# Kernel optimization log

Hardware: AMD Instinct MI355X
Metric: run time of the kernel (lower is better)

Reference implementation:

```python
import jax, jax.numpy as jnp
import numpy as np

HEADS = 16
EMB_DIM = 1024
MODEL_DIM = 1024
HEAD_DIM = EMB_DIM // HEADS
N, SEQ = 4, 1024


def setup_inputs() -> dict:
    key = jax.random.key(0)
    ks = jax.random.split(key, 9)
    s = 1.0 / np.sqrt(EMB_DIM)
    return {
        "query_inputs": jax.random.normal(ks[0], (N, SEQ, EMB_DIM), jnp.float32),
        "key_inputs": jax.random.normal(ks[1], (N, SEQ, EMB_DIM), jnp.float32),
        "value_inputs": jax.random.normal(ks[2], (N, SEQ, EMB_DIM), jnp.float32),
        "Wq": jax.random.normal(ks[3], (MODEL_DIM, EMB_DIM), jnp.float32) * s,
        "bq": jax.random.normal(ks[4], (MODEL_DIM,), jnp.float32) * s,
        "Wk": jax.random.normal(ks[5], (MODEL_DIM, EMB_DIM), jnp.float32) * s,
        "bk": jax.random.normal(ks[6], (MODEL_DIM,), jnp.float32) * s,
        "Wv": jax.random.normal(ks[7], (MODEL_DIM, EMB_DIM), jnp.float32) * s,
        "bv": jax.random.normal(ks[8], (MODEL_DIM,), jnp.float32) * s,
    }


def reference(query_inputs, key_inputs, value_inputs, Wq, bq, Wk, bk, Wv, bv):
    n = query_inputs.shape[0]
    qi = query_inputs.reshape(n, -1, query_inputs.shape[-1])
    ki = key_inputs.reshape(n, -1, key_inputs.shape[-1])
    vi = value_inputs.reshape(n, -1, value_inputs.shape[-1])
    q = qi @ Wq.T + bq  # (n, L, model_dim)
    k = ki @ Wk.T + bk
    v = vi @ Wv.T + bv
    L = q.shape[1]
    # Faithful to original (q/v swapped role): 'values'<-q, 'queries'<-v
    values = q.reshape(n, L, HEADS, HEAD_DIM)
    keys = k.reshape(n, L, HEADS, HEAD_DIM)
    queries = v.reshape(n, L, HEADS, HEAD_DIM)
    energy = jnp.einsum('nqhd,nkhd->nhqk', queries, keys)
    attention = jax.nn.softmax(energy / jnp.sqrt(jnp.float32(EMB_DIM)), axis=3)
    out = jnp.einsum('nhql,nlhd->nqhd', attention, values).reshape(n, L, HEADS * HEAD_DIM)
    return out
```

## Files before the change

### kernel.cpp

```cpp
#include <hip/hip_runtime.h>


typedef unsigned short u16;
typedef __attribute__((ext_vector_type(8))) short bf16x8;
typedef __attribute__((ext_vector_type(4))) float f32x4;

#define S_LEN 1024
#define EMB 1024
#define HEADS 16
#define HD 64

__device__ __forceinline__ u16 f2bf(float f) {
    unsigned int u = __float_as_uint(f);
    u = (u + 0x7fffu + ((u >> 16) & 1u)) >> 16;
    return (u16)u;
}

typedef const __attribute__((address_space(1))) unsigned glob_u32;
typedef __attribute__((address_space(3))) unsigned lds_u32;
__device__ __forceinline__ void gld16(const u16* g, u16* l) {
    __builtin_amdgcn_global_load_lds((glob_u32*)g, (lds_u32*)l, 16, 0, 0);
}

struct CvtArgs {
    const float* src[6];
    u16* dst[6];
};

__global__ __launch_bounds__(256) void cvt_f32_bf16(CvtArgs a)
{
    const long total = (3L << 20) + (3L << 18);
    for (long i = (long)blockIdx.x * 256 + threadIdx.x; i < total;
         i += (long)gridDim.x * 256) {
        int arr, off;
        if (i < (3L << 20)) { arr = (int)(i >> 20); off = (int)(i & ((1 << 20) - 1)); }
        else { long j = i - (3L << 20); arr = 3 + (int)(j >> 18); off = (int)(j & ((1 << 18) - 1)); }
        float4 v = reinterpret_cast<const float4*>(a.src[arr])[off];
        ushort4 o; o.x = f2bf(v.x); o.y = f2bf(v.y); o.z = f2bf(v.z); o.w = f2bf(v.w);
        reinterpret_cast<ushort4*>(a.dst[arr])[off] = o;
    }
}

__global__ __launch_bounds__(256) void qkv_gemm_bf16(
    const u16* __restrict__ Xq, const u16* __restrict__ Xk, const u16* __restrict__ Xv,
    const u16* __restrict__ Wq, const u16* __restrict__ Wk, const u16* __restrict__ Wv,
    const float* __restrict__ Bq, const float* __restrict__ Bk, const float* __restrict__ Bv,
    u16* __restrict__ vt, u16* __restrict__ katt, u16* __restrict__ qatt)
{
    const int proj = blockIdx.z;
    const u16* X  = (proj == 0) ? Xq : (proj == 1) ? Xk : Xv;
    const u16* W  = (proj == 0) ? Wq : (proj == 1) ? Wk : Wv;
    const float* Bp = (proj == 0) ? Bq : (proj == 1) ? Bk : Bv;

    const int gm0 = blockIdx.x * 128;
    const int gn0 = blockIdx.y * 128;
    const int tid  = threadIdx.x;
    const int lane = tid & 63;
    const int wave = tid >> 6;
    const int wm = wave >> 1, wn = wave & 1;
    const int l15 = lane & 15, l4 = lane >> 4;

    __shared__ u16 As[128 * 32];
    __shared__ u16 Bs[128 * 32];

    f32x4 acc[4][4];
    #pragma unroll
    for (int i = 0; i < 4; ++i)
        #pragma unroll
        for (int j = 0; j < 4; ++j) { f32x4 z = {0.f,0.f,0.f,0.f}; acc[i][j] = z; }

    const int r0 = tid >> 2,        cc0 = tid & 3;
    const int r1 = (tid + 256) >> 2, cc1 = (tid + 256) & 3;
    const u16* gA0 = X + (size_t)(gm0 + r0) * EMB + cc0 * 8;
    const u16* gA1 = X + (size_t)(gm0 + r1) * EMB + cc1 * 8;
    const u16* gB0 = W + (size_t)(gn0 + r0) * EMB + cc0 * 8;
    const u16* gB1 = W + (size_t)(gn0 + r1) * EMB + cc1 * 8;
    u16* lA0 = As + wave * 512;
    u16* lA1 = As + 2048 + wave * 512;
    u16* lB0 = Bs + wave * 512;
    u16* lB1 = Bs + 2048 + wave * 512;

    for (int kt = 0; kt < 32; ++kt) {
        const int k0 = kt * 32;
        gld16(gA0 + k0, lA0);
        gld16(gA1 + k0, lA1);
        gld16(gB0 + k0, lB0);
        gld16(gB1 + k0, lB1);
        __syncthreads();

        bf16x8 af[4], bfr[4];
        #pragma unroll
        for (int m = 0; m < 4; ++m)
            af[m] = *reinterpret_cast<const bf16x8*>(&As[(wm * 64 + m * 16 + l15) * 32 + l4 * 8]);
        #pragma unroll
        for (int n = 0; n < 4; ++n)
            bfr[n] = *reinterpret_cast<const bf16x8*>(&Bs[(wn * 64 + n * 16 + l15) * 32 + l4 * 8]);

        #pragma unroll
        for (int m = 0; m < 4; ++m)
            #pragma unroll
            for (int n = 0; n < 4; ++n)
                acc[m][n] = __builtin_amdgcn_mfma_f32_16x16x32_bf16(af[m], bfr[n], acc[m][n], 0, 0, 0);
        __syncthreads();
    }

    #pragma unroll
    for (int n = 0; n < 4; ++n) {
        const int col = gn0 + wn * 64 + n * 16 + l15;
        const float bias = Bp[col];
        const int h = col >> 6, d = col & 63;
        #pragma unroll
        for (int m = 0; m < 4; ++m) {
            #pragma unroll
            for (int r = 0; r < 4; ++r) {
                const int rowg = gm0 + wm * 64 + m * 16 + l4 * 4 + r;
                const int nb = rowg >> 10, s = rowg & 1023;
                const u16 val = f2bf(acc[m][n][r] + bias);
                const int nh = nb * HEADS + h;
                if (proj == 0)       vt  [((size_t)nh * HD + d) * S_LEN + s] = val;
                else if (proj == 1)  katt[((size_t)nh * S_LEN + s) * HD + d] = val;
                else                 qatt[((size_t)nh * S_LEN + s) * HD + d] = val;
            }
        }
    }
}

__global__ __launch_bounds__(256) void qkv_gemm_f32(
    const float* __restrict__ Xq, const float* __restrict__ Xk, const float* __restrict__ Xv,
    const float* __restrict__ Wq, const float* __restrict__ Wk, const float* __restrict__ Wv,
    const float* __restrict__ Bq, const float* __restrict__ Bk, const float* __restrict__ Bv,
    u16* __restrict__ vt, u16* __restrict__ katt, u16* __restrict__ qatt)
{
    const int proj = blockIdx.z;
    const float* X = (proj == 0) ? Xq : (proj == 1) ? Xk : Xv;
    const float* W = (proj == 0) ? Wq : (proj == 1) ? Wk : Wv;
    const float* Bp = (proj == 0) ? Bq : (proj == 1) ? Bk : Bv;

    const int gm0 = blockIdx.x * 128;
    const int gn0 = blockIdx.y * 128;
    const int tid  = threadIdx.x;
    const int lane = tid & 63;
    const int wave = tid >> 6;
    const int wm = wave >> 1, wn = wave & 1;
    const int l15 = lane & 15, l4 = lane >> 4;

    __shared__ u16 As[128 * 40];
    __shared__ u16 Bs[128 * 40];

    f32x4 acc[4][4];
    #pragma unroll
    for (int i = 0; i < 4; ++i)
        #pragma unroll
        for (int j = 0; j < 4; ++j) { f32x4 z = {0.f,0.f,0.f,0.f}; acc[i][j] = z; }

    const int srow = tid >> 3;
    const int skc  = (tid & 7) * 4;

    for (int kt = 0; kt < 32; ++kt) {
        const int k0 = kt * 32;
        #pragma unroll
        for (int p = 0; p < 4; ++p) {
            const int row = p * 32 + srow;
            float4 a = *reinterpret_cast<const float4*>(&X[(size_t)(gm0 + row) * EMB + k0 + skc]);
            float4 b = *reinterpret_cast<const float4*>(&W[(size_t)(gn0 + row) * EMB + k0 + skc]);
            ushort4 ua; ua.x = f2bf(a.x); ua.y = f2bf(a.y); ua.z = f2bf(a.z); ua.w = f2bf(a.w);
            ushort4 ub; ub.x = f2bf(b.x); ub.y = f2bf(b.y); ub.z = f2bf(b.z); ub.w = f2bf(b.w);
            *reinterpret_cast<ushort4*>(&As[row * 40 + skc]) = ua;
            *reinterpret_cast<ushort4*>(&Bs[row * 40 + skc]) = ub;
        }
        __syncthreads();

        bf16x8 af[4], bfr[4];
        #pragma unroll
        for (int m = 0; m < 4; ++m)
            af[m] = *reinterpret_cast<const bf16x8*>(&As[(wm * 64 + m * 16 + l15) * 40 + l4 * 8]);
        #pragma unroll
        for (int n = 0; n < 4; ++n)
            bfr[n] = *reinterpret_cast<const bf16x8*>(&Bs[(wn * 64 + n * 16 + l15) * 40 + l4 * 8]);

        #pragma unroll
        for (int m = 0; m < 4; ++m)
            #pragma unroll
            for (int n = 0; n < 4; ++n)
                acc[m][n] = __builtin_amdgcn_mfma_f32_16x16x32_bf16(af[m], bfr[n], acc[m][n], 0, 0, 0);
        __syncthreads();
    }

    #pragma unroll
    for (int n = 0; n < 4; ++n) {
        const int col = gn0 + wn * 64 + n * 16 + l15;
        const float bias = Bp[col];
        const int h = col >> 6, d = col & 63;
        #pragma unroll
        for (int m = 0; m < 4; ++m) {
            #pragma unroll
            for (int r = 0; r < 4; ++r) {
                const int rowg = gm0 + wm * 64 + m * 16 + l4 * 4 + r;
                const int nb = rowg >> 10, s = rowg & 1023;
                const u16 val = f2bf(acc[m][n][r] + bias);
                const int nh = nb * HEADS + h;
                if (proj == 0)       vt  [((size_t)nh * HD + d) * S_LEN + s] = val;
                else if (proj == 1)  katt[((size_t)nh * S_LEN + s) * HD + d] = val;
                else                 qatt[((size_t)nh * S_LEN + s) * HD + d] = val;
            }
        }
    }
}

__global__ __launch_bounds__(256) void attn_kernel(
    const u16* __restrict__ qatt, const u16* __restrict__ katt,
    const u16* __restrict__ vt, float* __restrict__ out)
{
    const int qb = blockIdx.x;
    const int nh = blockIdx.y;
    const int tid  = threadIdx.x;
    const int lane = tid & 63;
    const int wave = tid >> 6;
    const int l15 = lane & 15, l4 = lane >> 4;
    const int q0 = qb * 64;
    const int waveQ = wave * 16;

    __shared__ u16 Ks[2][64 * 64];
    __shared__ u16 Vs[2][64 * 64];
    __shared__ u16 Ps[4 * 16 * 72];

    const size_t qbase = (size_t)nh * S_LEN * HD + (size_t)(q0 + waveQ + l15) * HD;
    const bf16x8 qf0 = *reinterpret_cast<const bf16x8*>(&qatt[qbase + l4 * 8]);
    const bf16x8 qf1 = *reinterpret_cast<const bf16x8*>(&qatt[qbase + 32 + l4 * 8]);

    const int r8  = lane >> 3;
    const int ccg = (lane & 7) ^ r8;
    const int row0 = wave * 8 + r8;
    const int row1 = 32 + row0;
    const u16* gK = katt + (size_t)nh * S_LEN * HD;
    const u16* gV = vt   + (size_t)nh * HD * S_LEN;
    const u16* gK0 = gK + (size_t)row0 * HD + ccg * 8;
    const u16* gK1 = gK + (size_t)row1 * HD + ccg * 8;
    const u16* gV0 = gV + (size_t)row0 * S_LEN + ccg * 8;
    const u16* gV1 = gV + (size_t)row1 * S_LEN + ccg * 8;

    f32x4 accO[4];
    #pragma unroll
    for (int i = 0; i < 4; ++i) { f32x4 z = {0.f,0.f,0.f,0.f}; accO[i] = z; }
    float lsum[4] = {0.f, 0.f, 0.f, 0.f};
    const float scale = 0.03125f;

    {
        u16* kb = &Ks[0][0] + wave * 512;
        u16* vb = &Vs[0][0] + wave * 512;
        gld16(gK0, kb);          gld16(gK1, kb + 2048);
        gld16(gV0, vb);          gld16(gV1, vb + 2048);
    }
    __syncthreads();

    for (int kt = 0; kt < 16; ++kt) {
        const int cur = kt & 1;
        if (kt < 15) {
            const size_t kOff = (size_t)(kt + 1) * 64 * HD;
            const size_t vOff = (size_t)(kt + 1) * 64;
            u16* kb = &Ks[cur ^ 1][0] + wave * 512;
            u16* vb = &Vs[cur ^ 1][0] + wave * 512;
            gld16(gK0 + kOff, kb);       gld16(gK1 + kOff, kb + 2048);
            gld16(gV0 + vOff, vb);       gld16(gV1 + vOff, vb + 2048);
        }

        char* KsB = reinterpret_cast<char*>(&Ks[cur][0]);
        char* VsB = reinterpret_cast<char*>(&Vs[cur][0]);

        float pvals[4][4];
        #pragma unroll
        for (int kb = 0; kb < 4; ++kb) {
            const int krow = kb * 16 + l15;
            const int sw = krow & 7;
            bf16x8 kf0 = *reinterpret_cast<const bf16x8*>(KsB + krow * 128 + ((l4 ^ sw) << 4));
            bf16x8 kf1 = *reinterpret_cast<const bf16x8*>(KsB + krow * 128 + (((l4 + 4) ^ sw) << 4));
            f32x4 sacc = {0.f, 0.f, 0.f, 0.f};
            sacc = __builtin_amdgcn_mfma_f32_16x16x32_bf16(qf0, kf0, sacc, 0, 0, 0);
            sacc = __builtin_amdgcn_mfma_f32_16x16x32_bf16(qf1, kf1, sacc, 0, 0, 0);
            #pragma unroll
            for (int r = 0; r < 4; ++r) {
                const float pv = __expf(sacc[r] * scale);
                pvals[kb][r] = pv;
                lsum[r] += pv;
            }
        }

        u16* pw = &Ps[wave * 16 * 72];
        #pragma unroll
        for (int r = 0; r < 4; ++r) {
            const int prow = l4 * 4 + r;
            #pragma unroll
            for (int kb = 0; kb < 4; ++kb)
                pw[prow * 72 + kb * 16 + l15] = f2bf(pvals[kb][r]);
        }
        asm volatile("s_waitcnt lgkmcnt(0)" ::: "memory");
        __builtin_amdgcn_sched_barrier(0);

        const u16* pr = &Ps[wave * 16 * 72 + l15 * 72];
        const bf16x8 pf0 = *reinterpret_cast<const bf16x8*>(&pr[l4 * 8]);
        const bf16x8 pf1 = *reinterpret_cast<const bf16x8*>(&pr[32 + l4 * 8]);

        #pragma unroll
        for (int db = 0; db < 4; ++db) {
            const int vrow = db * 16 + l15;
            const int sw = vrow & 7;
            bf16x8 vf0 = *reinterpret_cast<const bf16x8*>(VsB + vrow * 128 + ((l4 ^ sw) << 4));
            bf16x8 vf1 = *reinterpret_cast<const bf16x8*>(VsB + vrow * 128 + (((l4 + 4) ^ sw) << 4));
            accO[db] = __builtin_amdgcn_mfma_f32_16x16x32_bf16(pf0, vf0, accO[db], 0, 0, 0);
            accO[db] = __builtin_amdgcn_mfma_f32_16x16x32_bf16(pf1, vf1, accO[db], 0, 0, 0);
        }
        __syncthreads();
    }

    #pragma unroll
    for (int r = 0; r < 4; ++r) {
        float s = lsum[r];
        #pragma unroll
        for (int msk = 1; msk < 16; msk <<= 1) s += __shfl_xor(s, msk);
        lsum[r] = 1.0f / s;
    }

    const int n = nh >> 4, h = nh & 15;
    #pragma unroll
    for (int db = 0; db < 4; ++db) {
        const int d = h * 64 + db * 16 + l15;
        #pragma unroll
        for (int r = 0; r < 4; ++r) {
            const int s = q0 + waveQ + l4 * 4 + r;
            out[(size_t)n * S_LEN * EMB + (size_t)s * EMB + d] = accO[db][r] * lsum[r];
        }
    }
}

extern "C" void kernel_launch(void* const* d_in, const int* in_sizes, int n_in,
                              void* d_out, int out_size, void* d_ws, size_t ws_size,
                              hipStream_t stream)
{
    const float* Xq = (const float*)d_in[0];
    const float* Xk = (const float*)d_in[1];
    const float* Xv = (const float*)d_in[2];
    const float* Wq = (const float*)d_in[3];
    const float* bq = (const float*)d_in[4];
    const float* Wk = (const float*)d_in[5];
    const float* bk = (const float*)d_in[6];
    const float* Wv = (const float*)d_in[7];
    const float* bv = (const float*)d_in[8];
    float* out = (float*)d_out;

    const size_t M4 = (size_t)4 * 1024 * 1024;
    const size_t M1 = (size_t)1024 * 1024;

    u16* vt   = (u16*)d_ws;
    u16* katt = vt + M4;
    u16* qatt = katt + M4;

    const size_t need = (3 * M4 + 3 * M4 + 3 * M1) * sizeof(u16);

    if (ws_size >= need) {
        u16* Xqb = qatt + M4;
        u16* Xkb = Xqb + M4;
        u16* Xvb = Xkb + M4;
        u16* Wqb = Xvb + M4;
        u16* Wkb = Wqb + M1;
        u16* Wvb = Wkb + M1;

        CvtArgs ca;
        ca.src[0] = Xq; ca.src[1] = Xk; ca.src[2] = Xv;
        ca.src[3] = Wq; ca.src[4] = Wk; ca.src[5] = Wv;
        ca.dst[0] = Xqb; ca.dst[1] = Xkb; ca.dst[2] = Xvb;
        ca.dst[3] = Wqb; ca.dst[4] = Wkb; ca.dst[5] = Wvb;
        cvt_f32_bf16<<<2048, 256, 0, stream>>>(ca);

        qkv_gemm_bf16<<<dim3(32, 8, 3), 256, 0, stream>>>(
            Xqb, Xkb, Xvb, Wqb, Wkb, Wvb, bq, bk, bv, vt, katt, qatt);
    } else {
        qkv_gemm_f32<<<dim3(32, 8, 3), 256, 0, stream>>>(
            Xq, Xk, Xv, Wq, Wk, Wv, bq, bk, bv, vt, katt, qatt);
    }

    attn_kernel<<<dim3(16, 64), 256, 0, stream>>>(qatt, katt, vt, out);
}
```

Baseline: 199.0 us.

## Multi-buffer the QKV projection GEMM with a four-stage LDS ring

Replaces the single-buffered load-sync-compute loop of the projection GEMM with a four-slot LDS ring. Three k-tiles are prefetched ahead through direct global-to-LDS loads, and explicit vmcnt waits plus raw barriers replace the paired __syncthreads. The goal is to hide global load latency behind the MFMA work. In exchange, LDS use per block grows fourfold to 64KB, which may lower occupancy.

```diff
diff --git a/kernel.cpp b/kernel.cpp
--- a/kernel.cpp
+++ b/kernel.cpp
@@ -60,8 +60,8 @@
     const int wm = wave >> 1, wn = wave & 1;
     const int l15 = lane & 15, l4 = lane >> 4;
 
-    __shared__ u16 As[128 * 32];
-    __shared__ u16 Bs[128 * 32];
+    __shared__ u16 As[4][128 * 32];
+    __shared__ u16 Bs[4][128 * 32];
 
     f32x4 acc[4][4];
     #pragma unroll
@@ -69,40 +69,56 @@
         #pragma unroll
         for (int j = 0; j < 4; ++j) { f32x4 z = {0.f,0.f,0.f,0.f}; acc[i][j] = z; }
 
-    const int r0 = tid >> 2,        cc0 = tid & 3;
+    const int r0 = tid >> 2,         cc0 = tid & 3;
     const int r1 = (tid + 256) >> 2, cc1 = (tid + 256) & 3;
     const u16* gA0 = X + (size_t)(gm0 + r0) * EMB + cc0 * 8;
     const u16* gA1 = X + (size_t)(gm0 + r1) * EMB + cc1 * 8;
     const u16* gB0 = W + (size_t)(gn0 + r0) * EMB + cc0 * 8;
     const u16* gB1 = W + (size_t)(gn0 + r1) * EMB + cc1 * 8;
-    u16* lA0 = As + wave * 512;
-    u16* lA1 = As + 2048 + wave * 512;
-    u16* lB0 = Bs + wave * 512;
-    u16* lB1 = Bs + 2048 + wave * 512;
-
-    for (int kt = 0; kt < 32; ++kt) {
-        const int k0 = kt * 32;
-        gld16(gA0 + k0, lA0);
-        gld16(gA1 + k0, lA1);
-        gld16(gB0 + k0, lB0);
-        gld16(gB1 + k0, lB1);
-        __syncthreads();
-
+
+    auto stage = [&](int buf, int ktile) {
+        const int k0 = ktile * 32;
+        u16* a = &As[buf][0] + wave * 512;
+        u16* b = &Bs[buf][0] + wave * 512;
+        gld16(gA0 + k0, a);
+        gld16(gA1 + k0, a + 2048);
+        gld16(gB0 + k0, b);
+        gld16(gB1 + k0, b + 2048);
+    };
+
+    auto compute = [&](int kt) {
+        const u16* A = &As[kt & 3][0];
+        const u16* B = &Bs[kt & 3][0];
         bf16x8 af[4], bfr[4];
         #pragma unroll
         for (int m = 0; m < 4; ++m)
-            af[m] = *reinterpret_cast<const bf16x8*>(&As[(wm * 64 + m * 16 + l15) * 32 + l4 * 8]);
+            af[m] = *reinterpret_cast<const bf16x8*>(&A[(wm * 64 + m * 16 + l15) * 32 + l4 * 8]);
         #pragma unroll
         for (int n = 0; n < 4; ++n)
-            bfr[n] = *reinterpret_cast<const bf16x8*>(&Bs[(wn * 64 + n * 16 + l15) * 32 + l4 * 8]);
-
+            bfr[n] = *reinterpret_cast<const bf16x8*>(&B[(wn * 64 + n * 16 + l15) * 32 + l4 * 8]);
         #pragma unroll
         for (int m = 0; m < 4; ++m)
             #pragma unroll
             for (int n = 0; n < 4; ++n)
                 acc[m][n] = __builtin_amdgcn_mfma_f32_16x16x32_bf16(af[m], bfr[n], acc[m][n], 0, 0, 0);
-        __syncthreads();
-    }
+    };
+
+    stage(0, 0);
+    stage(1, 1);
+    stage(2, 2);
+
+    for (int kt = 0; kt < 30; ++kt) {
+        asm volatile("s_waitcnt vmcnt(8)" ::: "memory");
+        __builtin_amdgcn_s_barrier();
+        if (kt <= 28) stage((kt + 3) & 3, kt + 3);
+        compute(kt);
+    }
+    asm volatile("s_waitcnt vmcnt(4)" ::: "memory");
+    __builtin_amdgcn_s_barrier();
+    compute(30);
+    asm volatile("s_waitcnt vmcnt(0)" ::: "memory");
+    __builtin_amdgcn_s_barrier();
+    compute(31);
 
     #pragma unroll
     for (int n = 0; n < 4; ++n) {
```

New measurement: 215.2 us. +8.1%, slower.
